# Performance work log

Measured on AMD Instinct MI355X. Metric: run time of the kernel, lower is better.

The kernel has to match this reference:

```python
import jax, jax.numpy as jnp
import numpy as np

B, T, E, H, D = 4, 2048, 1024, 16, 64  # batch, seq (==context), embed, heads, head_size


def setup_inputs() -> dict:
    key = jax.random.key(0)
    ks = jax.random.split(key, 5)
    s_in = 1.0 / np.sqrt(E)
    s_c = 1.0 / np.sqrt(H * D)
    return {
        "x": jax.random.normal(ks[0], (B, T, E), dtype=jnp.float32),
        "Wq": jax.random.normal(ks[1], (H, E, D), dtype=jnp.float32) * s_in,
        "Wk": jax.random.normal(ks[2], (H, E, D), dtype=jnp.float32) * s_in,
        "Wv": jax.random.normal(ks[3], (H, E, D), dtype=jnp.float32) * s_in,
        "Wc": jax.random.normal(ks[4], (H * D, E), dtype=jnp.float32) * s_c,
    }


def reference(x, Wq, Wk, Wv, Wc):
    # Batched equivalent of the per-head Python loop: each head h does
    # q = x @ Wq[h], k = x @ Wk[h], v = x @ Wv[h]; causal softmax attention.
    q = jnp.einsum("bse,hed->bhsd", x, Wq)
    k = jnp.einsum("bte,hed->bhtd", x, Wk)
    v = jnp.einsum("bte,hed->bhtd", x, Wv)
    scale = 1.0 / jnp.sqrt(jnp.asarray(D, dtype=x.dtype))
    scores = jnp.einsum("bhsd,bhtd->bhst", q, k) * scale  # [B,H,T,T]
    causal = jnp.tril(jnp.ones((T, T), dtype=bool))
    scores = jnp.where(causal[None, None], scores, jnp.asarray(-jnp.inf, dtype=scores.dtype))
    attn = jax.nn.softmax(scores, axis=-1)
    out = jnp.einsum("bhst,bhtd->bhsd", attn, v)
    # concat heads along last dim (head 0 first), then combine linear
    out = out.transpose(0, 2, 1, 3).reshape(B, T, H * D)
    return out @ Wc
```

## Files before the change

### kernel.cpp

```cpp
#include <hip/hip_runtime.h>
#include <cstdint>
#include <cstddef>

typedef unsigned short u16;
typedef __bf16 bf16x8 __attribute__((ext_vector_type(8)));
typedef float f32x4 __attribute__((ext_vector_type(4)));
typedef float f32x16 __attribute__((ext_vector_type(16)));

#define B_ 4
#define T_ 2048
#define E_ 1024
#define H_ 16
#define D_ 64
#define HD3_ 3072
#define M_ (B_*T_)

#if __has_builtin(__builtin_amdgcn_exp2f)
#define EXP2F(x) __builtin_amdgcn_exp2f(x)
#else
#define EXP2F(x) exp2f(x)
#endif
#if __has_builtin(__builtin_amdgcn_rcpf)
#define RCPF(x) __builtin_amdgcn_rcpf(x)
#else
#define RCPF(x) (1.f/(x))
#endif

__device__ __forceinline__ u16 f2bf(float f) {
  union { float f; unsigned u; } v; v.f = f;
  unsigned r = v.u + 0x7FFFu + ((v.u >> 16) & 1u);
  return (u16)(r >> 16);
}

__device__ __forceinline__ unsigned cvtpk(float a, float b) {
  unsigned r;
  asm("v_cvt_pk_bf16_f32 %0, %1, %2" : "=v"(r) : "v"(a), "v"(b));
  return r;
}

__device__ __forceinline__ void gl2lds16(const u16* g, u16* l) {
  __builtin_amdgcn_global_load_lds(
      (const __attribute__((address_space(1))) unsigned int*)g,
      (__attribute__((address_space(3))) unsigned int*)l, 16, 0, 0);
}

__global__ void prep_x(const float* __restrict__ x, u16* __restrict__ xb) {
  const long n4 = (long)(M_) * E_ / 4;
  for (long i = (long)blockIdx.x * blockDim.x + threadIdx.x; i < n4;
       i += (long)gridDim.x * blockDim.x) {
    float4 v = ((const float4*)x)[i];
    unsigned lo = (unsigned)f2bf(v.x) | ((unsigned)f2bf(v.y) << 16);
    unsigned hi = (unsigned)f2bf(v.z) | ((unsigned)f2bf(v.w) << 16);
    ((uint2*)xb)[i] = make_uint2(lo, hi);
  }
}

__global__ void prep_w(const float* __restrict__ Wq, const float* __restrict__ Wk,
                       const float* __restrict__ Wv, const float* __restrict__ Wc,
                       u16* __restrict__ WT, u16* __restrict__ WcT) {
  const int total = HD3_ * E_ + E_ * E_;
  for (int i = blockIdx.x * blockDim.x + threadIdx.x; i < total;
       i += gridDim.x * blockDim.x) {
    if (i < HD3_ * E_) {
      int n = i >> 10, e = i & 1023;
      int mtx = n >> 10, hd = n & 1023, h = hd >> 6, d = hd & 63;
      const float* W = (mtx == 0) ? Wq : (mtx == 1) ? Wk : Wv;
      WT[i] = f2bf(W[((size_t)h * E_ + e) * D_ + d]);
    } else {
      int j = i - HD3_ * E_;
      int n = j >> 10, k = j & 1023;
      WcT[j] = f2bf(Wc[(size_t)k * E_ + n]);
    }
  }
}

template<int N_, bool OUT_BF16>
__global__ __launch_bounds__(512, 2) void gemm8(
    const u16* __restrict__ A, const u16* __restrict__ Bt,
    void* __restrict__ Cv, float qscale)
{
  __shared__ u16 As[2][128 * 64];
  __shared__ u16 Bs[2][256 * 64];
  const int tid = threadIdx.x;
  const int lane = tid & 63, w = tid >> 6;
  const int wr = w >> 2, wc = w & 3;
  const int l15 = lane & 15, l4 = lane >> 4;

  const int gx = N_ / 256;
  const int lin = blockIdx.x;
  const int cpx = (gx * 64) >> 3;
  const int swz = (lin & 7) * cpx + (lin >> 3);
  const int bxi = swz % gx, byi = swz / gx;
  const size_t bm = (size_t)byi * 128, bn = (size_t)bxi * 256;
  const u16* Ag = A + bm * 1024;
  const u16* Bg = Bt + bn * 1024;

  auto stageA = [&](int b, int t, int i) {
    int idx = i * 512 + tid, r = idx >> 3, c = idx & 7;
    gl2lds16(Ag + (size_t)r * 1024 + t * 64 + ((c ^ (r & 7)) * 8), &As[b][idx * 8]);
  };
  auto stageB = [&](int b, int t, int i) {
    int idx = i * 512 + tid, r = idx >> 3, c = idx & 7;
    gl2lds16(Bg + (size_t)r * 1024 + t * 64 + ((c ^ (r & 7)) * 8), &Bs[b][idx * 8]);
  };

  int aoff[4][2], boff[4][2];
#pragma unroll
  for (int m = 0; m < 4; ++m) {
    int r = wr * 64 + m * 16 + l15;
#pragma unroll
    for (int s = 0; s < 2; ++s)
      aoff[m][s] = r * 64 + (((s * 4 + l4) ^ (r & 7)) * 8);
  }
#pragma unroll
  for (int n = 0; n < 4; ++n) {
    int r = wc * 64 + n * 16 + l15;
#pragma unroll
    for (int s = 0; s < 2; ++s)
      boff[n][s] = r * 64 + (((s * 4 + l4) ^ (r & 7)) * 8);
  }

  f32x4 acc[4][4] = {};

#pragma unroll
  for (int i = 0; i < 2; ++i) stageA(0, 0, i);
#pragma unroll
  for (int i = 0; i < 4; ++i) stageB(0, 0, i);
#pragma unroll
  for (int i = 0; i < 2; ++i) stageA(1, 1, i);
  asm volatile("s_waitcnt vmcnt(2)" ::: "memory");
  __builtin_amdgcn_s_barrier();

  for (int t = 0; t < 16; ++t) {
    const int cur = t & 1;
    bf16x8 af[4][2], bfv[4][2];
#pragma unroll
    for (int m = 0; m < 4; ++m)
#pragma unroll
      for (int s = 0; s < 2; ++s)
        af[m][s] = *(const bf16x8*)&As[cur][aoff[m][s]];
#pragma unroll
    for (int n = 0; n < 2; ++n)
#pragma unroll
      for (int s = 0; s < 2; ++s)
        bfv[n][s] = *(const bf16x8*)&Bs[cur][boff[n][s]];
    if (t + 1 < 16) {
      stageB(cur ^ 1, t + 1, 0);
      stageB(cur ^ 1, t + 1, 1);
      stageB(cur ^ 1, t + 1, 2);
    }
    __builtin_amdgcn_s_barrier();
    asm volatile("s_waitcnt lgkmcnt(0)" ::: "memory");
    __builtin_amdgcn_sched_barrier(0);
    __builtin_amdgcn_s_setprio(1);
#pragma unroll
    for (int m = 0; m < 4; ++m)
#pragma unroll
      for (int n = 0; n < 2; ++n)
#pragma unroll
        for (int s = 0; s < 2; ++s)
          acc[m][n] = __builtin_amdgcn_mfma_f32_16x16x32_bf16(
              af[m][s], bfv[n][s], acc[m][n], 0, 0, 0);
    __builtin_amdgcn_s_setprio(0);
    __builtin_amdgcn_s_barrier();

#pragma unroll
    for (int n = 2; n < 4; ++n)
#pragma unroll
      for (int s = 0; s < 2; ++s)
        bfv[n][s] = *(const bf16x8*)&Bs[cur][boff[n][s]];
    if (t + 1 < 16) stageB(cur ^ 1, t + 1, 3);
    if (t + 2 < 16) { stageA(cur, t + 2, 0); stageA(cur, t + 2, 1); }
    __builtin_amdgcn_s_barrier();
    asm volatile("s_waitcnt lgkmcnt(0)" ::: "memory");
    __builtin_amdgcn_sched_barrier(0);
    __builtin_amdgcn_s_setprio(1);
#pragma unroll
    for (int m = 0; m < 4; ++m)
#pragma unroll
      for (int n = 2; n < 4; ++n)
#pragma unroll
        for (int s = 0; s < 2; ++s)
          acc[m][n] = __builtin_amdgcn_mfma_f32_16x16x32_bf16(
              af[m][s], bfv[n][s], acc[m][n], 0, 0, 0);
    __builtin_amdgcn_s_setprio(0);
    if (t + 2 < 16)      asm volatile("s_waitcnt vmcnt(2)" ::: "memory");
    else if (t + 1 < 16) asm volatile("s_waitcnt vmcnt(0)" ::: "memory");
    __builtin_amdgcn_s_barrier();
  }

#pragma unroll
  for (int m = 0; m < 4; ++m)
#pragma unroll
    for (int n = 0; n < 4; ++n) {
      size_t row = bm + wr * 64 + m * 16 + l4 * 4;
      size_t col = bn + wc * 64 + n * 16 + l15;
      float sc = (col < 1024) ? qscale : 1.0f;
#pragma unroll
      for (int j = 0; j < 4; ++j) {
        if (OUT_BF16)
          ((u16*)Cv)[(row + j) * N_ + col] = f2bf(acc[m][n][j] * sc);
        else
          ((float*)Cv)[(row + j) * N_ + col] = acc[m][n][j];
      }
    }
}

__global__ __launch_bounds__(256) void transpose_v(const u16* __restrict__ QKV,
                                                   u16* __restrict__ VT) {
  const int bh = blockIdx.y, b = bh >> 4, h = bh & 15;
  const int t0 = blockIdx.x * 64;
  __shared__ u16 tile[64][72];
  const int tid = threadIdx.x;
  const u16* src = QKV + ((size_t)(b * T_ + t0) * HD3_ + 2048 + h * 64);
#pragma unroll
  for (int i = 0; i < 2; ++i) {
    int c = i * 256 + tid;
    int r = c >> 3, cc = (c & 7) * 8;
    uint4 v = *(const uint4*)(src + (size_t)r * HD3_ + cc);
    *(uint4*)&tile[r][cc] = v;
  }
  __syncthreads();
  u16* dst = VT + (size_t)bh * D_ * T_ + t0;
#pragma unroll
  for (int i = 0; i < 16; ++i) {
    int idx = i * 256 + tid;
    int d = idx >> 6, tl = idx & 63;
    dst[(size_t)d * T_ + tl] = tile[tl][d];
  }
}

__global__ __launch_bounds__(256, 4) void attn_kernel(
    const u16* __restrict__ QKV, const u16* __restrict__ VT,
    u16* __restrict__ O)
{
  __shared__ u16 Ks[2][4096];
  __shared__ u16 Vs[2][4096];
  const int L = blockIdx.x;
  const int bh = L & 63, b = bh >> 4, h = bh & 15;
  const int jj = L >> 8, gg = (L >> 6) & 3;
  const int qt = 4 * jj + ((gg + jj) & 3);
  const int q0 = qt * 128;
  const int tid = threadIdx.x, w = tid >> 6, lane = tid & 63;
  const int ql = lane & 31, hi = lane >> 5;
  const int qw0 = q0 + w * 32;

  const u16* Qg = QKV + ((size_t)(b * T_ + q0) * HD3_ + h * 64);
  const u16* Kg = QKV + ((size_t)(b * T_) * HD3_ + 1024 + h * 64);
  const u16* Vg = VT + (size_t)bh * (D_ * T_);

#pragma unroll
  for (int i = 0; i < 4; ++i) {
    int c = i * 256 + tid, r = c >> 3, cc = c & 7, sc = cc ^ (r & 7);
    gl2lds16(Qg + (size_t)r * HD3_ + sc * 8, &Ks[0][0] + c * 8);
  }
  __syncthreads();
  bf16x8 qf[4];
  {
    int qrow = w * 32 + ql;
#pragma unroll
    for (int s = 0; s < 4; ++s) {
      int ch = (2 * s + hi) ^ (qrow & 7);
      qf[s] = *(const bf16x8*)(&Ks[0][0] + qrow * 64 + ch * 8);
    }
  }
  __syncthreads();

  int koff[2][4];
#pragma unroll
  for (int f = 0; f < 2; ++f) {
    int row = f * 32 + ql, swzr = row & 7;
#pragma unroll
    for (int s = 0; s < 4; ++s)
      koff[f][s] = row * 64 + (((2 * s + hi) ^ swzr) * 8);
  }

  const int c0 = tid, c1 = 256 + tid;
  const int r0_ = c0 >> 3, sc0 = (c0 & 7) ^ (r0_ & 7);
  const int r1_ = c1 >> 3, sc1 = (c1 & 7) ^ (r1_ & 7);
  const int lo0 = c0 * 8, lo1 = c1 * 8;
  const u16* kp0 = Kg + (size_t)r0_ * HD3_ + sc0 * 8;
  const u16* kp1 = Kg + (size_t)r1_ * HD3_ + sc1 * 8;
  const u16* vp0 = Vg + (size_t)r0_ * T_ + sc0 * 8;
  const u16* vp1 = Vg + (size_t)r1_ * T_ + sc1 * 8;

  gl2lds16(kp0, &Ks[0][lo0]);
  gl2lds16(kp1, &Ks[0][lo1]);
  gl2lds16(vp0, &Vs[0][lo0]);
  gl2lds16(vp1, &Vs[0][lo1]);
  kp0 += 64 * HD3_; kp1 += 64 * HD3_;
  vp0 += 64; vp1 += 64;

  f32x16 acc[2];
#pragma unroll
  for (int ni = 0; ni < 2; ++ni)
#pragma unroll
    for (int r = 0; r < 16; ++r) acc[ni][r] = 0.f;
  float mrun = -1e30f, lrun = 0.f;
  const int ktmax = 2 * qt + 2;

  for (int kt = 0; kt < ktmax; ++kt) {
    const int cur = kt & 1;
    const int kv0 = kt * 64;
    __syncthreads();
    if (kt + 1 < ktmax) {
      u16* kb = &Ks[cur ^ 1][0];
      u16* vb = &Vs[cur ^ 1][0];
      gl2lds16(kp0, kb + lo0);
      gl2lds16(kp1, kb + lo1);
      gl2lds16(vp0, vb + lo0);
      gl2lds16(vp1, vb + lo1);
      kp0 += 64 * HD3_; kp1 += 64 * HD3_;
      vp0 += 64; vp1 += 64;
    }
    if (kv0 > qw0 + 31) continue;
    const u16* kbase = &Ks[cur][0];
    const u16* vbase = &Vs[cur][0];

    f32x16 st[2];
#pragma unroll
    for (int f = 0; f < 2; ++f)
#pragma unroll
      for (int r = 0; r < 16; ++r) st[f][r] = 0.f;
    __builtin_amdgcn_s_setprio(1);
#pragma unroll
    for (int f = 0; f < 2; ++f)
#pragma unroll
      for (int s = 0; s < 4; ++s) {
        bf16x8 kfr = *(const bf16x8*)(kbase + koff[f][s]);
        st[f] = __builtin_amdgcn_mfma_f32_32x32x16_bf16(kfr, qf[s], st[f], 0, 0, 0);
      }
    __builtin_amdgcn_s_setprio(0);

    if (kv0 + 63 > qw0) {
      const int qg = qw0 + ql;
#pragma unroll
      for (int f = 0; f < 2; ++f)
#pragma unroll
        for (int r = 0; r < 16; ++r) {
          int kg = kv0 + f * 32 + (r & 3) + 8 * (r >> 2) + 4 * hi;
          if (kg > qg) st[f][r] = -1e30f;
        }
    }

    float tr[16];
#pragma unroll
    for (int r = 0; r < 16; ++r) tr[r] = fmaxf(st[0][r], st[1][r]);
#pragma unroll
    for (int ss = 8; ss; ss >>= 1)
#pragma unroll
      for (int r = 0; r < 8; ++r)
        if (r < ss) tr[r] = fmaxf(tr[r], tr[r + ss]);
    float mt = fmaxf(tr[0], __shfl_xor(tr[0], 32, 64));
    if (!__all(mt - mrun <= 8.f)) {
      float mnew = fmaxf(mrun, mt);
      float corr = EXP2F(mrun - mnew);
      lrun *= corr;
#pragma unroll
      for (int ni = 0; ni < 2; ++ni)
#pragma unroll
        for (int r = 0; r < 16; ++r) acc[ni][r] *= corr;
      mrun = mnew;
    }

#pragma unroll
    for (int f = 0; f < 2; ++f)
#pragma unroll
      for (int r = 0; r < 16; ++r) st[f][r] = EXP2F(st[f][r] - mrun);
#pragma unroll
    for (int r = 0; r < 16; ++r) tr[r] = st[0][r] + st[1][r];
#pragma unroll
    for (int ss = 8; ss; ss >>= 1)
#pragma unroll
      for (int r = 0; r < 8; ++r)
        if (r < ss) tr[r] += tr[r + ss];
    lrun += tr[0] + __shfl_xor(tr[0], 32, 64);

    __builtin_amdgcn_s_setprio(1);
#pragma unroll
    for (int s = 0; s < 4; ++s) {
      const int f = s >> 1, bse = (s & 1) * 8;
      unsigned b0 = cvtpk(st[f][bse + 0], st[f][bse + 1]);
      unsigned b1 = cvtpk(st[f][bse + 2], st[f][bse + 3]);
      unsigned a0 = cvtpk(st[f][bse + 4], st[f][bse + 5]);
      unsigned a1 = cvtpk(st[f][bse + 6], st[f][bse + 7]);
      asm volatile("v_permlane32_swap_b32 %0, %1" : "+v"(b0), "+v"(a0));
      asm volatile("v_permlane32_swap_b32 %0, %1" : "+v"(b1), "+v"(a1));
      union { unsigned u[4]; bf16x8 v; } pa;
      pa.u[0] = b0; pa.u[1] = b1; pa.u[2] = a0; pa.u[3] = a1;
#pragma unroll
      for (int ni = 0; ni < 2; ++ni) {
        bf16x8 vf = *(const bf16x8*)(vbase + koff[ni][s]);
        acc[ni] = __builtin_amdgcn_mfma_f32_32x32x16_bf16(vf, pa.v, acc[ni], 0, 0, 0);
      }
    }
    __builtin_amdgcn_s_setprio(0);
  }

  const int q = q0 + w * 32 + ql;
  u16* Og = O + ((size_t)(b * T_ + q) * (H_ * D_) + h * 64);
  const float inv = RCPF(lrun);
#pragma unroll
  for (int ni = 0; ni < 2; ++ni)
#pragma unroll
    for (int rr = 0; rr < 8; ++rr) {
      const int r0 = rr * 2;
      const int d0 = ((r0 & 3) + 8 * (r0 >> 2)) + 4 * hi + ni * 32;
      unsigned pk = cvtpk(acc[ni][r0] * inv, acc[ni][r0 + 1] * inv);
      *(unsigned*)(Og + d0) = pk;
    }
}

extern "C" void kernel_launch(void* const* d_in, const int* in_sizes, int n_in,
                              void* d_out, int out_size, void* d_ws, size_t ws_size,
                              hipStream_t stream) {
  const float* x  = (const float*)d_in[0];
  const float* Wq = (const float*)d_in[1];
  const float* Wk = (const float*)d_in[2];
  const float* Wv = (const float*)d_in[3];
  const float* Wc = (const float*)d_in[4];

  char* ws = (char*)d_ws;
  u16* xb  = (u16*)(ws);
  u16* WT  = (u16*)(ws + 16777216);
  u16* WcT = (u16*)(ws + 23068672);
  u16* QKV = (u16*)(ws + 25165824);
  u16* Ob  = (u16*)(ws + 75497472);
  u16* VT  = xb;
  float* out = (float*)d_out;

  const float QSCALE = 0.125f * 1.4426950408889634f;

  prep_x<<<2048, 256, 0, stream>>>(x, xb);
  prep_w<<<4096, 256, 0, stream>>>(Wq, Wk, Wv, Wc, WT, WcT);
  gemm8<3072, true><<<768, 512, 0, stream>>>(xb, WT, QKV, QSCALE);
  transpose_v<<<dim3(32, 64), 256, 0, stream>>>(QKV, VT);
  attn_kernel<<<dim3(1024), 256, 0, stream>>>(QKV, VT, Ob);
  gemm8<1024, false><<<256, 512, 0, stream>>>(Ob, WcT, out, 1.0f);
}
```

Baseline: 260.2 us.

## Tile weight prep and V transpose through LDS with vectorized coalesced stores

Rewrites prep_w as a 64x64 LDS-tiled transpose that reads float4 rows and writes 16-byte packed bf16 rows, replacing strided per-element gathers. It also folds the Q softmax scale into the bf16 weights so the QKV GEMM epilogue no longer multiplies per column. transpose_v gets the same vectorized 16-byte store pattern in place of scalar 2-byte stores. The intent is to cut uncoalesced global traffic in the prep kernels. Rounding Q weights after scaling changes numerics slightly.

Measured after the change: 253.3 us. 2.6% less time.

```diff
diff --git a/kernel.cpp b/kernel.cpp
--- a/kernel.cpp
+++ b/kernel.cpp
@@ -55,29 +55,52 @@
   }
 }
 
-__global__ void prep_w(const float* __restrict__ Wq, const float* __restrict__ Wk,
-                       const float* __restrict__ Wv, const float* __restrict__ Wc,
-                       u16* __restrict__ WT, u16* __restrict__ WcT) {
-  const int total = HD3_ * E_ + E_ * E_;
-  for (int i = blockIdx.x * blockDim.x + threadIdx.x; i < total;
-       i += gridDim.x * blockDim.x) {
-    if (i < HD3_ * E_) {
-      int n = i >> 10, e = i & 1023;
-      int mtx = n >> 10, hd = n & 1023, h = hd >> 6, d = hd & 63;
-      const float* W = (mtx == 0) ? Wq : (mtx == 1) ? Wk : Wv;
-      WT[i] = f2bf(W[((size_t)h * E_ + e) * D_ + d]);
-    } else {
-      int j = i - HD3_ * E_;
-      int n = j >> 10, k = j & 1023;
-      WcT[j] = f2bf(Wc[(size_t)k * E_ + n]);
-    }
+__global__ __launch_bounds__(256) void prep_w(
+    const float* __restrict__ Wq, const float* __restrict__ Wk,
+    const float* __restrict__ Wv, const float* __restrict__ Wc,
+    u16* __restrict__ WT, u16* __restrict__ WcT, float qscale)
+{
+  __shared__ u16 tile[64][72];
+  const int id = blockIdx.x;
+  const int tid = threadIdx.x, lane = tid & 63;
+  const float* src; int srcStride; u16* dst; float scale = 1.f;
+  if (id < 768) {
+    int mtxh = id >> 4, et = id & 15;
+    int mtx = mtxh >> 4, h = mtxh & 15;
+    const float* W = (mtx == 0) ? Wq : (mtx == 1) ? Wk : Wv;
+    src = W + (size_t)h * 65536 + (size_t)(et * 64) * 64;
+    srcStride = 64;
+    dst = WT + (size_t)(mtx * 1024 + h * 64) * 1024 + et * 64;
+    if (mtx == 0) scale = qscale;
+  } else {
+    int j = id - 768;
+    int kt = j >> 4, nt = j & 15;
+    src = Wc + (size_t)(kt * 64) * 1024 + nt * 64;
+    srcStride = 1024;
+    dst = WcT + (size_t)(nt * 64) * 1024 + kt * 64;
+  }
+#pragma unroll
+  for (int i = 0; i < 4; ++i) {
+    int u = i * 256 + tid, r = u >> 4, c4 = (u & 15) * 4;
+    float4 v = *(const float4*)(src + (size_t)r * srcStride + c4);
+    *(uint2*)&tile[r][c4] = make_uint2(
+        (unsigned)f2bf(v.x * scale) | ((unsigned)f2bf(v.y * scale) << 16),
+        (unsigned)f2bf(v.z * scale) | ((unsigned)f2bf(v.w * scale) << 16));
+  }
+  __syncthreads();
+#pragma unroll
+  for (int i = 0; i < 2; ++i) {
+    int grp = i * 4 + (tid >> 6);
+    u16 tmp[8];
+#pragma unroll
+    for (int j = 0; j < 8; ++j) tmp[j] = tile[grp * 8 + j][lane];
+    *(uint4*)(dst + (size_t)lane * 1024 + grp * 8) = *(uint4*)tmp;
   }
 }
 
 template<int N_, bool OUT_BF16>
 __global__ __launch_bounds__(512, 2) void gemm8(
-    const u16* __restrict__ A, const u16* __restrict__ Bt,
-    void* __restrict__ Cv, float qscale)
+    const u16* __restrict__ A, const u16* __restrict__ Bt, void* __restrict__ Cv)
 {
   __shared__ u16 As[2][128 * 64];
   __shared__ u16 Bs[2][256 * 64];
@@ -195,11 +218,10 @@
     for (int n = 0; n < 4; ++n) {
       size_t row = bm + wr * 64 + m * 16 + l4 * 4;
       size_t col = bn + wc * 64 + n * 16 + l15;
-      float sc = (col < 1024) ? qscale : 1.0f;
 #pragma unroll
       for (int j = 0; j < 4; ++j) {
         if (OUT_BF16)
-          ((u16*)Cv)[(row + j) * N_ + col] = f2bf(acc[m][n][j] * sc);
+          ((u16*)Cv)[(row + j) * N_ + col] = f2bf(acc[m][n][j]);
         else
           ((float*)Cv)[(row + j) * N_ + col] = acc[m][n][j];
       }
@@ -211,22 +233,22 @@
   const int bh = blockIdx.y, b = bh >> 4, h = bh & 15;
   const int t0 = blockIdx.x * 64;
   __shared__ u16 tile[64][72];
-  const int tid = threadIdx.x;
+  const int tid = threadIdx.x, lane = tid & 63;
   const u16* src = QKV + ((size_t)(b * T_ + t0) * HD3_ + 2048 + h * 64);
 #pragma unroll
   for (int i = 0; i < 2; ++i) {
-    int c = i * 256 + tid;
-    int r = c >> 3, cc = (c & 7) * 8;
-    uint4 v = *(const uint4*)(src + (size_t)r * HD3_ + cc);
-    *(uint4*)&tile[r][cc] = v;
+    int c = i * 256 + tid, r = c >> 3, cc = (c & 7) * 8;
+    *(uint4*)&tile[r][cc] = *(const uint4*)(src + (size_t)r * HD3_ + cc);
   }
   __syncthreads();
-  u16* dst = VT + (size_t)bh * D_ * T_ + t0;
-#pragma unroll
-  for (int i = 0; i < 16; ++i) {
-    int idx = i * 256 + tid;
-    int d = idx >> 6, tl = idx & 63;
-    dst[(size_t)d * T_ + tl] = tile[tl][d];
+  u16* dst = VT + (size_t)bh * (D_ * T_) + t0;
+#pragma unroll
+  for (int i = 0; i < 2; ++i) {
+    int grp = i * 4 + (tid >> 6);
+    u16 tmp[8];
+#pragma unroll
+    for (int j = 0; j < 8; ++j) tmp[j] = tile[grp * 8 + j][lane];
+    *(uint4*)(dst + (size_t)lane * T_ + grp * 8) = *(uint4*)tmp;
   }
 }
 
@@ -362,7 +384,6 @@
         for (int r = 0; r < 16; ++r) acc[ni][r] *= corr;
       mrun = mnew;
     }
-
 #pragma unroll
     for (int f = 0; f < 2; ++f)
 #pragma unroll
@@ -432,9 +453,9 @@
   const float QSCALE = 0.125f * 1.4426950408889634f;
 
   prep_x<<<2048, 256, 0, stream>>>(x, xb);
-  prep_w<<<4096, 256, 0, stream>>>(Wq, Wk, Wv, Wc, WT, WcT);
-  gemm8<3072, true><<<768, 512, 0, stream>>>(xb, WT, QKV, QSCALE);
+  prep_w<<<1024, 256, 0, stream>>>(Wq, Wk, Wv, Wc, WT, WcT, QSCALE);
+  gemm8<3072, true><<<768, 512, 0, stream>>>(xb, WT, QKV);
   transpose_v<<<dim3(32, 64), 256, 0, stream>>>(QKV, VT);
   attn_kernel<<<dim3(1024), 256, 0, stream>>>(QKV, VT, Ob);
-  gemm8<1024, false><<<256, 512, 0, stream>>>(Ob, WcT, out, 1.0f);
-}
+  gemm8<1024, false><<<256, 512, 0, stream>>>(Ob, WcT, out);
+}
```
